# Optimization experiments

Measured on AMD Instinct MI355X. Metric: run time of the kernel, lower is better.

The kernel has to match this reference:

```python
import jax, jax.numpy as jnp
import numpy as np

B, S, D = 2, 2048, 512
H, HD = 8, 64  # num_heads, head_size; all_head_size = H*HD = 512


def setup_inputs() -> dict:
    key = jax.random.key(0)
    ks = jax.random.split(key, 11)
    sc = 0.02
    return {
        "query": jax.random.normal(ks[0], (B, S, D), jnp.float32),
        "key": jax.random.normal(ks[1], (B, S, D), jnp.float32),
        "value": jax.random.normal(ks[2], (B, S, D), jnp.float32),
        "Wq": jax.random.normal(ks[3], (D, H * HD), jnp.float32) * sc,
        "bq": jnp.zeros((H * HD,), jnp.float32),
        "Wk": jax.random.normal(ks[4], (D, H * HD), jnp.float32) * sc,
        "bk": jnp.zeros((H * HD,), jnp.float32),
        "Wv": jax.random.normal(ks[5], (D, H * HD), jnp.float32) * sc,
        "bv": jnp.zeros((H * HD,), jnp.float32),
        "Wo": jax.random.normal(ks[6], (H * HD, D), jnp.float32) * sc,
        "bo": jnp.zeros((D,), jnp.float32),
    }


def _split_heads(x):
    b, s, _ = x.shape
    return x.reshape(b, s, H, HD).transpose(0, 2, 1, 3)  # [B,H,S,HD]


def reference(query, key, value, Wq, bq, Wk, bk, Wv, bv, Wo, bo):
    q = _split_heads(query @ Wq + bq)
    k = _split_heads(key @ Wk + bk)
    v = _split_heads(value @ Wv + bv)
    scores = jnp.einsum("bhqd,bhkd->bhqk", q, k) / jnp.sqrt(jnp.asarray(HD, q.dtype))
    probs = jax.nn.softmax(scores, axis=-1)  # dropout rate 0.0, inference
    ctx = jnp.einsum("bhqk,bhkd->bhqd", probs, v)
    ctx = ctx.transpose(0, 2, 1, 3).reshape(query.shape[0], -1, H * HD)
    return ctx @ Wo + bo
```

## Files before the change

kernel.cpp:

```cpp
#include <hip/hip_runtime.h>
#include <math.h>

#define BATCH 2
#define SEQ 2048
#define DMODEL 512
#define NH 8
#define HDIM 64
#define MTOT (BATCH * SEQ)
#define QSIZE (BATCH * NH * SEQ * HDIM)
#define WSIZE (DMODEL * DMODEL)

typedef __attribute__((ext_vector_type(8))) short bf16x8;
typedef __attribute__((ext_vector_type(4))) float f32x4;

__device__ inline unsigned short f2bf(float f) {
    union { float f; unsigned u; } v; v.f = f;
    unsigned u = v.u;
    u += 0x7fffu + ((u >> 16) & 1u);
    return (unsigned short)(u >> 16);
}
__device__ inline unsigned pack2(float lo, float hi) {
    unsigned r;
    asm("v_cvt_pk_bf16_f32 %0, %1, %2" : "=v"(r) : "v"(lo), "v"(hi));
    return r;
}

#define LSTR 72

#define WS_Q   ((size_t)0)
#define WS_K   ((size_t)QSIZE)
#define WS_V   (2 * (size_t)QSIZE)
#define WS_CTX (3 * (size_t)QSIZE)
#define WS_WT  (4 * (size_t)QSIZE)
#define WS_ABF (4 * (size_t)QSIZE + 4 * (size_t)WSIZE)

__global__ __launch_bounds__(256) void wt_prep_kernel(
    const float* __restrict__ Wq, const float* __restrict__ Wk,
    const float* __restrict__ Wv, const float* __restrict__ Wo,
    unsigned short* __restrict__ wt)
{
    const int z = blockIdx.z;
    const float* W = (z == 0) ? Wq : (z == 1) ? Wk : (z == 2) ? Wv : Wo;
    unsigned short* Wt = wt + (size_t)z * WSIZE;

    __shared__ float T[32][33];
    const int tid = threadIdx.x;
    const int k0 = blockIdx.x * 32, n0 = blockIdx.y * 32;

    {
        int r = tid >> 3, c = (tid & 7) * 4;
        float4 v = *(const float4*)&W[(size_t)(k0 + r) * DMODEL + n0 + c];
        T[r][c + 0] = v.x; T[r][c + 1] = v.y; T[r][c + 2] = v.z; T[r][c + 3] = v.w;
    }
    __syncthreads();
    {
        int n = tid >> 3, c = (tid & 7) * 4;
        uint2 o;
        o.x = pack2(T[c + 0][n], T[c + 1][n]);
        o.y = pack2(T[c + 2][n], T[c + 3][n]);
        *(uint2*)&Wt[(size_t)(n0 + n) * DMODEL + k0 + c] = o;
    }
}

__global__ __launch_bounds__(256) void inp_prep_kernel(
    const float* __restrict__ qin, const float* __restrict__ kin,
    const float* __restrict__ vin, unsigned short* __restrict__ abf)
{
    const int z = blockIdx.y;
    const float* src = (z == 0) ? qin : (z == 1) ? kin : vin;
    unsigned short* dst = abf + (size_t)z * QSIZE;

    const size_t i = ((size_t)blockIdx.x * 256 + threadIdx.x) * 8;
    float4 f0 = *(const float4*)(src + i);
    float4 f1 = *(const float4*)(src + i + 4);
    uint4 o;
    o.x = pack2(f0.x, f0.y); o.y = pack2(f0.z, f0.w);
    o.z = pack2(f1.x, f1.y); o.w = pack2(f1.z, f1.w);
    *(uint4*)(dst + i) = o;
}

__global__ __launch_bounds__(256) void qkv_mfma_kernel(
    unsigned short* __restrict__ ws,
    const float* __restrict__ bq, const float* __restrict__ bk,
    const float* __restrict__ bv)
{
    const int which = blockIdx.z;
    const unsigned short* A  = ws + WS_ABF + (size_t)which * QSIZE;
    const unsigned short* Wt = ws + WS_WT + (size_t)which * WSIZE;
    const float* bias = (which == 0) ? bq : (which == 1) ? bk : bv;
    unsigned short* out = ws + (size_t)which * QSIZE;

    __shared__ __align__(16) short As[128][LSTR];
    __shared__ __align__(16) short Bs[128][LSTR];

    const int tid = threadIdx.x;
    const int lane = tid & 63, wave = tid >> 6;
    const int lrow = lane & 15, quad = lane >> 4;
    const int m0 = blockIdx.y * 128, n0 = blockIdx.x * 128;

    const int sr = tid >> 1;
    const int sh = (tid & 1) * 32;

    f32x4 acc[2][8];
    #pragma unroll
    for (int i = 0; i < 2; ++i)
        #pragma unroll
        for (int n = 0; n < 8; ++n) acc[i][n] = f32x4{0.f, 0.f, 0.f, 0.f};

    for (int k0 = 0; k0 < DMODEL; k0 += 64) {
        __syncthreads();
        {
            const unsigned short* ap = A + (size_t)(m0 + sr) * DMODEL + k0 + sh;
            uint4 a0 = *(const uint4*)(ap + 0),  a1 = *(const uint4*)(ap + 8);
            uint4 a2 = *(const uint4*)(ap + 16), a3 = *(const uint4*)(ap + 24);
            *(uint4*)&As[sr][sh + 0]  = a0;
            *(uint4*)&As[sr][sh + 8]  = a1;
            *(uint4*)&As[sr][sh + 16] = a2;
            *(uint4*)&As[sr][sh + 24] = a3;
        }
        {
            const unsigned short* wp = Wt + (size_t)(n0 + sr) * DMODEL + k0 + sh;
            uint4 b0 = *(const uint4*)(wp + 0),  b1 = *(const uint4*)(wp + 8);
            uint4 b2 = *(const uint4*)(wp + 16), b3 = *(const uint4*)(wp + 24);
            *(uint4*)&Bs[sr][sh + 0]  = b0;
            *(uint4*)&Bs[sr][sh + 8]  = b1;
            *(uint4*)&Bs[sr][sh + 16] = b2;
            *(uint4*)&Bs[sr][sh + 24] = b3;
        }
        __syncthreads();
        #pragma unroll
        for (int s = 0; s < 2; ++s) {
            bf16x8 af[2];
            #pragma unroll
            for (int i = 0; i < 2; ++i)
                af[i] = *(const bf16x8*)&As[wave * 32 + i * 16 + lrow][s * 32 + quad * 8];
            #pragma unroll
            for (int n = 0; n < 8; ++n) {
                bf16x8 bf = *(const bf16x8*)&Bs[n * 16 + lrow][s * 32 + quad * 8];
                acc[0][n] = __builtin_amdgcn_mfma_f32_16x16x32_bf16(af[0], bf, acc[0][n], 0, 0, 0);
                acc[1][n] = __builtin_amdgcn_mfma_f32_16x16x32_bf16(af[1], bf, acc[1][n], 0, 0, 0);
            }
        }
    }

    if (which < 2) {
        const float scale = (which == 0) ? 0.125f : 1.0f;
        #pragma unroll
        for (int n = 0; n < 8; ++n) {
            const int col = n0 + n * 16 + lrow;
            const int h_ = col >> 6, hd_ = col & 63;
            const float bv_ = bias[col];
            #pragma unroll
            for (int i = 0; i < 2; ++i) {
                #pragma unroll
                for (int r = 0; r < 4; ++r) {
                    const int m = m0 + wave * 32 + i * 16 + quad * 4 + r;
                    const int b_ = m >> 11, s_ = m & (SEQ - 1);
                    const float v = (acc[i][n][r] + bv_) * scale;
                    out[((size_t)((b_ * NH + h_) * SEQ + s_)) * HDIM + hd_] = f2bf(v);
                }
            }
        }
    } else {
        #pragma unroll
        for (int n = 0; n < 8; ++n) {
            const int col = n0 + n * 16 + lrow;
            const int h_ = col >> 6, hd_ = col & 63;
            const float bv_ = bias[col];
            #pragma unroll
            for (int i = 0; i < 2; ++i) {
                const int m = m0 + wave * 32 + i * 16 + quad * 4;
                const int b_ = m >> 11, s_ = m & (SEQ - 1);
                uint2 o;
                o.x = pack2(acc[i][n][0] + bv_, acc[i][n][1] + bv_);
                o.y = pack2(acc[i][n][2] + bv_, acc[i][n][3] + bv_);
                *(uint2*)&out[((size_t)((b_ * NH + h_) * HDIM + hd_)) * SEQ + s_] = o;
            }
        }
    }
}

#define HSEQ (SEQ / 2)
#define OSTR 68

__global__ __launch_bounds__(512) void attn_mfma_kernel(
    const unsigned short* __restrict__ ws, unsigned short* __restrict__ ctx)
{
    const unsigned short* Q = ws + WS_Q;
    const unsigned short* K = ws + WS_K;
    const unsigned short* V = ws + WS_V;

    __shared__ __align__(16) short Ks[2][64][LSTR];
    __shared__ __align__(16) short Vt[2][64][LSTR];
    __shared__ __align__(16) short Ps[2][64][LSTR];

    const int bh = blockIdx.x;
    const int q0 = blockIdx.y * 64;
    const int tid = threadIdx.x;
    const int lane = tid & 63, wave = tid >> 6;
    const int half = wave >> 2, w4 = wave & 3;
    const int lrow = lane & 15, quad = lane >> 4;
    const size_t base = (size_t)bh * SEQ * HDIM;

    const unsigned short* qrow = Q + base + (size_t)(q0 + w4 * 16 + lrow) * HDIM;
    const bf16x8 qb0 = *(const bf16x8*)(qrow + quad * 8);
    const bf16x8 qb1 = *(const bf16x8*)(qrow + 32 + quad * 8);

    float m_prev = -1e30f, l_run = 0.f;
    f32x4 oacc[4];
    #pragma unroll
    for (int n = 0; n < 4; ++n) oacc[n] = f32x4{0.f, 0.f, 0.f, 0.f};

    const int t = tid & 255;
    const int kr = t >> 2, kc = (t & 3) * 16;
    const int ktbase = half * HSEQ;

    for (int kt = 0; kt < HSEQ; kt += 64) {
        __syncthreads();
        {
            const unsigned short* kp = K + base + (size_t)(ktbase + kt + kr) * HDIM + kc;
            uint4 k0 = *(const uint4*)kp;
            uint4 k1 = *(const uint4*)(kp + 8);
            *(uint4*)&Ks[half][kr][kc]     = k0;
            *(uint4*)&Ks[half][kr][kc + 8] = k1;
        }
        {
            const unsigned short* vp = V + base + (size_t)kr * SEQ + ktbase + kt + kc;
            uint4 v0 = *(const uint4*)vp;
            uint4 v1 = *(const uint4*)(vp + 8);
            *(uint4*)&Vt[half][kr][kc]     = v0;
            *(uint4*)&Vt[half][kr][kc + 8] = v1;
        }
        __syncthreads();

        f32x4 st[4];
        #pragma unroll
        for (int n = 0; n < 4; ++n) {
            bf16x8 ka0 = *(const bf16x8*)&Ks[half][n * 16 + lrow][quad * 8];
            bf16x8 ka1 = *(const bf16x8*)&Ks[half][n * 16 + lrow][32 + quad * 8];
            f32x4 z = f32x4{0.f, 0.f, 0.f, 0.f};
            z = __builtin_amdgcn_mfma_f32_16x16x32_bf16(ka0, qb0, z, 0, 0, 0);
            z = __builtin_amdgcn_mfma_f32_16x16x32_bf16(ka1, qb1, z, 0, 0, 0);
            st[n] = z;
        }

        float tmax = st[0][0];
        #pragma unroll
        for (int n = 0; n < 4; ++n)
            #pragma unroll
            for (int r = 0; r < 4; ++r) tmax = fmaxf(tmax, st[n][r]);
        tmax = fmaxf(tmax, __shfl_xor(tmax, 16));
        tmax = fmaxf(tmax, __shfl_xor(tmax, 32));

        if (!__all(tmax <= m_prev + 8.f)) {
            const float mnew = fmaxf(m_prev, tmax);
            const float alpha = __expf(m_prev - mnew);
            l_run *= alpha;
            #pragma unroll
            for (int n = 0; n < 4; ++n) {
                oacc[n][0] *= alpha; oacc[n][1] *= alpha;
                oacc[n][2] *= alpha; oacc[n][3] *= alpha;
            }
            m_prev = mnew;
        }

        float p[4][4];
        float tsum = 0.f;
        #pragma unroll
        for (int n = 0; n < 4; ++n)
            #pragma unroll
            for (int r = 0; r < 4; ++r) {
                p[n][r] = __expf(st[n][r] - m_prev);
                tsum += p[n][r];
            }
        tsum += __shfl_xor(tsum, 16);
        tsum += __shfl_xor(tsum, 32);
        l_run += tsum;

        #pragma unroll
        for (int n = 0; n < 4; ++n) {
            uint2 o;
            o.x = pack2(p[n][0], p[n][1]);
            o.y = pack2(p[n][2], p[n][3]);
            *(uint2*)&Ps[half][w4 * 16 + lrow][n * 16 + quad * 4] = o;
        }

        bf16x8 pb0 = *(const bf16x8*)&Ps[half][w4 * 16 + lrow][quad * 8];
        bf16x8 pb1 = *(const bf16x8*)&Ps[half][w4 * 16 + lrow][32 + quad * 8];
        #pragma unroll
        for (int n = 0; n < 4; ++n) {
            bf16x8 va0 = *(const bf16x8*)&Vt[half][n * 16 + lrow][quad * 8];
            bf16x8 va1 = *(const bf16x8*)&Vt[half][n * 16 + lrow][32 + quad * 8];
            oacc[n] = __builtin_amdgcn_mfma_f32_16x16x32_bf16(va0, pb0, oacc[n], 0, 0, 0);
            oacc[n] = __builtin_amdgcn_mfma_f32_16x16x32_bf16(va1, pb1, oacc[n], 0, 0, 0);
        }
    }

    __syncthreads();
    float* Obuf = (float*)&Ks[0][0][0];
    float* Mbuf = (float*)&Ps[0][0][0];

    if (half == 1) {
        float* ob = Obuf + (size_t)w4 * (16 * OSTR) + (size_t)lrow * OSTR;
        #pragma unroll
        for (int n = 0; n < 4; ++n)
            *(f32x4*)&ob[n * 16 + quad * 4] = oacc[n];
        if (quad == 0) {
            Mbuf[w4 * 16 + lrow]      = m_prev;
            Mbuf[64 + w4 * 16 + lrow] = l_run;
        }
    }
    __syncthreads();
    if (half == 0) {
        const float m1 = Mbuf[w4 * 16 + lrow];
        const float l1 = Mbuf[64 + w4 * 16 + lrow];
        const float M  = fmaxf(m_prev, m1);
        const float a0 = __expf(m_prev - M), a1 = __expf(m1 - M);
        const float inv = 1.f / (l_run * a0 + l1 * a1);
        const float s0 = a0 * inv, s1 = a1 * inv;
        const float* ob = Obuf + (size_t)w4 * (16 * OSTR) + (size_t)lrow * OSTR;

        const int b_ = bh >> 3, h_ = bh & 7;
        const int qg = q0 + w4 * 16 + lrow;
        unsigned short* crow = ctx + ((size_t)(b_ * SEQ + qg)) * DMODEL + h_ * HDIM;
        #pragma unroll
        for (int n = 0; n < 4; ++n) {
            f32x4 o1 = *(const f32x4*)&ob[n * 16 + quad * 4];
            uint2 o;
            o.x = pack2(oacc[n][0] * s0 + o1[0] * s1, oacc[n][1] * s0 + o1[1] * s1);
            o.y = pack2(oacc[n][2] * s0 + o1[2] * s1, oacc[n][3] * s0 + o1[3] * s1);
            *(uint2*)&crow[n * 16 + quad * 4] = o;
        }
    }
}

__global__ __launch_bounds__(256) void out_proj_mfma_kernel(
    const unsigned short* __restrict__ ws, const float* __restrict__ bo,
    float* __restrict__ out)
{
    const unsigned short* ctx = ws + WS_CTX;
    const unsigned short* Wt  = ws + WS_WT + 3 * (size_t)WSIZE;

    __shared__ __align__(16) short As[128][LSTR];
    __shared__ __align__(16) short Bs[64][LSTR];

    const int tid = threadIdx.x;
    const int lane = tid & 63, wave = tid >> 6;
    const int lrow = lane & 15, quad = lane >> 4;
    const int m0 = blockIdx.y * 128, n0 = blockIdx.x * 64;

    const int sr = tid >> 1, sh = (tid & 1) * 32;
    const int br = tid >> 2, bqr = (tid & 3) * 16;

    f32x4 acc[2][4];
    #pragma unroll
    for (int i = 0; i < 2; ++i)
        #pragma unroll
        for (int n = 0; n < 4; ++n) acc[i][n] = f32x4{0.f, 0.f, 0.f, 0.f};

    for (int k0 = 0; k0 < DMODEL; k0 += 64) {
        __syncthreads();
        {
            const unsigned short* ap = ctx + (size_t)(m0 + sr) * DMODEL + k0 + sh;
            uint4 c0 = *(const uint4*)(ap + 0),  c1 = *(const uint4*)(ap + 8);
            uint4 c2 = *(const uint4*)(ap + 16), c3 = *(const uint4*)(ap + 24);
            *(uint4*)&As[sr][sh + 0]  = c0;
            *(uint4*)&As[sr][sh + 8]  = c1;
            *(uint4*)&As[sr][sh + 16] = c2;
            *(uint4*)&As[sr][sh + 24] = c3;
        }
        {
            const unsigned short* wp = Wt + (size_t)(n0 + br) * DMODEL + k0 + bqr;
            uint4 b0 = *(const uint4*)wp;
            uint4 b1 = *(const uint4*)(wp + 8);
            *(uint4*)&Bs[br][bqr]     = b0;
            *(uint4*)&Bs[br][bqr + 8] = b1;
        }
        __syncthreads();
        #pragma unroll
        for (int s = 0; s < 2; ++s) {
            bf16x8 af[2];
            #pragma unroll
            for (int i = 0; i < 2; ++i)
                af[i] = *(const bf16x8*)&As[wave * 32 + i * 16 + lrow][s * 32 + quad * 8];
            #pragma unroll
            for (int n = 0; n < 4; ++n) {
                bf16x8 bf = *(const bf16x8*)&Bs[n * 16 + lrow][s * 32 + quad * 8];
                acc[0][n] = __builtin_amdgcn_mfma_f32_16x16x32_bf16(af[0], bf, acc[0][n], 0, 0, 0);
                acc[1][n] = __builtin_amdgcn_mfma_f32_16x16x32_bf16(af[1], bf, acc[1][n], 0, 0, 0);
            }
        }
    }

    #pragma unroll
    for (int n = 0; n < 4; ++n) {
        const int col = n0 + n * 16 + lrow;
        const float bv_ = bo[col];
        #pragma unroll
        for (int i = 0; i < 2; ++i) {
            #pragma unroll
            for (int r = 0; r < 4; ++r) {
                const int m = m0 + wave * 32 + i * 16 + quad * 4 + r;
                out[(size_t)m * DMODEL + col] = acc[i][n][r] + bv_;
            }
        }
    }
}

extern "C" void kernel_launch(void* const* d_in, const int* in_sizes, int n_in,
                              void* d_out, int out_size, void* d_ws, size_t ws_size,
                              hipStream_t stream)
{
    const float* qin = (const float*)d_in[0];
    const float* kin = (const float*)d_in[1];
    const float* vin = (const float*)d_in[2];
    const float* Wq  = (const float*)d_in[3];
    const float* bq  = (const float*)d_in[4];
    const float* Wk  = (const float*)d_in[5];
    const float* bk  = (const float*)d_in[6];
    const float* Wv  = (const float*)d_in[7];
    const float* bv  = (const float*)d_in[8];
    const float* Wo  = (const float*)d_in[9];
    const float* bo  = (const float*)d_in[10];

    unsigned short* ws = (unsigned short*)d_ws;
    float* out = (float*)d_out;

    dim3 gw(DMODEL / 32, DMODEL / 32, 4);
    wt_prep_kernel<<<gw, 256, 0, stream>>>(Wq, Wk, Wv, Wo, ws + WS_WT);

    dim3 gi(QSIZE / (256 * 8), 3);
    inp_prep_kernel<<<gi, 256, 0, stream>>>(qin, kin, vin, ws + WS_ABF);

    dim3 gp(DMODEL / 128, MTOT / 128, 3);
    qkv_mfma_kernel<<<gp, 256, 0, stream>>>(ws, bq, bk, bv);

    dim3 ga(BATCH * NH, SEQ / 64);
    attn_mfma_kernel<<<ga, 512, 0, stream>>>(ws, ws + WS_CTX);

    dim3 go(DMODEL / 64, MTOT / 128);
    out_proj_mfma_kernel<<<go, 256, 0, stream>>>(ws, bo, out);
}
```

Baseline: 157.9 us.

## Double-buffer K/V tiles with register prefetch and keep P in registers

Double-buffers the attention kernel's K and V tiles in shared memory and prefetches the next tile into registers two steps ahead. This removes one of the two barriers per iteration and overlaps global loads with MFMA work. It drops the P round-trip through shared memory by permuting the V column layout so the packed probabilities can feed the PV MFMA straight from registers. It also adds s_setprio around the MFMA blocks and remaps block indices so that blocks sharing a head are grouped together. The cost is more registers and LDS per block, and the permuted layout must match the MFMA operand order exactly.

Result: faster. 147.7 us (-6.4%).

```diff
diff --git a/kernel.cpp b/kernel.cpp
--- a/kernel.cpp
+++ b/kernel.cpp
@@ -181,6 +181,7 @@
 }
 
 #define HSEQ (SEQ / 2)
+#define NT   (HSEQ / 64)
 #define OSTR 68
 
 __global__ __launch_bounds__(512) void attn_mfma_kernel(
@@ -190,12 +191,13 @@
     const unsigned short* K = ws + WS_K;
     const unsigned short* V = ws + WS_V;
 
-    __shared__ __align__(16) short Ks[2][64][LSTR];
-    __shared__ __align__(16) short Vt[2][64][LSTR];
-    __shared__ __align__(16) short Ps[2][64][LSTR];
-
-    const int bh = blockIdx.x;
-    const int q0 = blockIdx.y * 64;
+    __shared__ __align__(16) short Ks[2][2][64][LSTR];
+    __shared__ __align__(16) short Vt[2][2][64][LSTR];
+
+    const int lin = blockIdx.x + 16 * blockIdx.y;
+    const int bh  = (lin & 7) + 8 * (lin >> 8);
+    const int q0  = ((lin >> 3) & 31) * 64;
+
     const int tid = threadIdx.x;
     const int lane = tid & 63, wave = tid >> 6;
     const int half = wave >> 2, w4 = wave & 3;
@@ -211,38 +213,57 @@
     #pragma unroll
     for (int n = 0; n < 4; ++n) oacc[n] = f32x4{0.f, 0.f, 0.f, 0.f};
 
-    const int t = tid & 255;
-    const int kr = t >> 2, kc = (t & 3) * 16;
+    const int t  = tid & 255;
+    const int kr = t >> 2;
+    const int kc = (t & 3) * 16;
+    const int n_ = t & 3;
+    const int c0 = ((n_ >= 2) ? 32 : 0) + (n_ & 1) * 4;
     const int ktbase = half * HSEQ;
 
-    for (int kt = 0; kt < HSEQ; kt += 64) {
+    const unsigned short* kptr = K + base + (size_t)(ktbase + kr) * HDIM + kc;
+    const unsigned short* vptr = V + base + (size_t)kr * SEQ + ktbase + kc;
+
+    uint4 kA, kB, vA, vB;
+#define LOADT(TI) do { \
+        const unsigned short* kp = kptr + (size_t)(TI) * 64 * HDIM; \
+        const unsigned short* vp = vptr + (TI) * 64; \
+        kA = *(const uint4*)kp; kB = *(const uint4*)(kp + 8); \
+        vA = *(const uint4*)vp; vB = *(const uint4*)(vp + 8); \
+    } while (0)
+#define WRITET(BUF) do { \
+        *(uint4*)&Ks[half][BUF][kr][kc]     = kA; \
+        *(uint4*)&Ks[half][BUF][kr][kc + 8] = kB; \
+        uint2 w0; w0.x = vA.x; w0.y = vA.y; \
+        uint2 w1; w1.x = vA.z; w1.y = vA.w; \
+        uint2 w2; w2.x = vB.x; w2.y = vB.y; \
+        uint2 w3; w3.x = vB.z; w3.y = vB.w; \
+        *(uint2*)&Vt[half][BUF][kr][c0]      = w0; \
+        *(uint2*)&Vt[half][BUF][kr][c0 + 8]  = w1; \
+        *(uint2*)&Vt[half][BUF][kr][c0 + 16] = w2; \
+        *(uint2*)&Vt[half][BUF][kr][c0 + 24] = w3; \
+    } while (0)
+
+    LOADT(0);
+    WRITET(0);
+    LOADT(1);
+
+    #pragma unroll 2
+    for (int ti = 0; ti < NT; ++ti) {
+        const int cur = ti & 1;
         __syncthreads();
-        {
-            const unsigned short* kp = K + base + (size_t)(ktbase + kt + kr) * HDIM + kc;
-            uint4 k0 = *(const uint4*)kp;
-            uint4 k1 = *(const uint4*)(kp + 8);
-            *(uint4*)&Ks[half][kr][kc]     = k0;
-            *(uint4*)&Ks[half][kr][kc + 8] = k1;
-        }
-        {
-            const unsigned short* vp = V + base + (size_t)kr * SEQ + ktbase + kt + kc;
-            uint4 v0 = *(const uint4*)vp;
-            uint4 v1 = *(const uint4*)(vp + 8);
-            *(uint4*)&Vt[half][kr][kc]     = v0;
-            *(uint4*)&Vt[half][kr][kc + 8] = v1;
-        }
-        __syncthreads();
 
         f32x4 st[4];
+        __builtin_amdgcn_s_setprio(1);
         #pragma unroll
         for (int n = 0; n < 4; ++n) {
-            bf16x8 ka0 = *(const bf16x8*)&Ks[half][n * 16 + lrow][quad * 8];
-            bf16x8 ka1 = *(const bf16x8*)&Ks[half][n * 16 + lrow][32 + quad * 8];
+            bf16x8 ka0 = *(const bf16x8*)&Ks[half][cur][n * 16 + lrow][quad * 8];
+            bf16x8 ka1 = *(const bf16x8*)&Ks[half][cur][n * 16 + lrow][32 + quad * 8];
             f32x4 z = f32x4{0.f, 0.f, 0.f, 0.f};
             z = __builtin_amdgcn_mfma_f32_16x16x32_bf16(ka0, qb0, z, 0, 0, 0);
             z = __builtin_amdgcn_mfma_f32_16x16x32_bf16(ka1, qb1, z, 0, 0, 0);
             st[n] = z;
         }
+        __builtin_amdgcn_s_setprio(0);
 
         float tmax = st[0][0];
         #pragma unroll
@@ -277,28 +298,31 @@
         tsum += __shfl_xor(tsum, 32);
         l_run += tsum;
 
+        union { unsigned w[4]; bf16x8 v; } U0, U1;
+        U0.w[0] = pack2(p[0][0], p[0][1]); U0.w[1] = pack2(p[0][2], p[0][3]);
+        U0.w[2] = pack2(p[1][0], p[1][1]); U0.w[3] = pack2(p[1][2], p[1][3]);
+        U1.w[0] = pack2(p[2][0], p[2][1]); U1.w[1] = pack2(p[2][2], p[2][3]);
+        U1.w[2] = pack2(p[3][0], p[3][1]); U1.w[3] = pack2(p[3][2], p[3][3]);
+
+        __builtin_amdgcn_s_setprio(1);
         #pragma unroll
         for (int n = 0; n < 4; ++n) {
-            uint2 o;
-            o.x = pack2(p[n][0], p[n][1]);
-            o.y = pack2(p[n][2], p[n][3]);
-            *(uint2*)&Ps[half][w4 * 16 + lrow][n * 16 + quad * 4] = o;
-        }
-
-        bf16x8 pb0 = *(const bf16x8*)&Ps[half][w4 * 16 + lrow][quad * 8];
-        bf16x8 pb1 = *(const bf16x8*)&Ps[half][w4 * 16 + lrow][32 + quad * 8];
-        #pragma unroll
-        for (int n = 0; n < 4; ++n) {
-            bf16x8 va0 = *(const bf16x8*)&Vt[half][n * 16 + lrow][quad * 8];
-            bf16x8 va1 = *(const bf16x8*)&Vt[half][n * 16 + lrow][32 + quad * 8];
-            oacc[n] = __builtin_amdgcn_mfma_f32_16x16x32_bf16(va0, pb0, oacc[n], 0, 0, 0);
-            oacc[n] = __builtin_amdgcn_mfma_f32_16x16x32_bf16(va1, pb1, oacc[n], 0, 0, 0);
-        }
-    }
+            bf16x8 va0 = *(const bf16x8*)&Vt[half][cur][n * 16 + lrow][quad * 8];
+            bf16x8 va1 = *(const bf16x8*)&Vt[half][cur][n * 16 + lrow][32 + quad * 8];
+            oacc[n] = __builtin_amdgcn_mfma_f32_16x16x32_bf16(va0, U0.v, oacc[n], 0, 0, 0);
+            oacc[n] = __builtin_amdgcn_mfma_f32_16x16x32_bf16(va1, U1.v, oacc[n], 0, 0, 0);
+        }
+        __builtin_amdgcn_s_setprio(0);
+
+        if (ti < NT - 1) WRITET(cur ^ 1);
+        if (ti < NT - 2) LOADT(ti + 2);
+    }
+#undef LOADT
+#undef WRITET
 
     __syncthreads();
-    float* Obuf = (float*)&Ks[0][0][0];
-    float* Mbuf = (float*)&Ps[0][0][0];
+    float* Obuf = (float*)&Ks[0][0][0][0];
+    float* Mbuf = (float*)&Vt[0][0][0][0];
 
     if (half == 1) {
         float* ob = Obuf + (size_t)w4 * (16 * OSTR) + (size_t)lrow * OSTR;
```
